# Performance work log

Measured on AMD Instinct MI355X. Metric: run time of the kernel, lower is better.

The kernel has to match this reference:

```python
import jax, jax.numpy as jnp
import numpy as np

EPS = 1e-6
NEG_SLOPE = 0.2


def setup_inputs() -> dict:
    key = jax.random.key(0)
    k1, k2 = jax.random.split(key)
    B, D, T = 4, 512, 2048
    H, Dh = 8, 512 // 8
    x = jax.random.normal(k1, (B, D, T), dtype=jnp.float32)
    qkv = jax.random.normal(k2, (3, H, D, Dh), dtype=jnp.float32) * 0.02
    norm_w = jnp.ones((1,), dtype=jnp.float32)
    return {"x": x, "qkv": qkv, "norm_w": norm_w}


def reference(x, qkv, norm_w):
    B, D, T = x.shape
    H = qkv.shape[1]
    # leaky relu on channels-first input
    x = jnp.where(x >= 0, x, NEG_SLOPE * x)
    # fused QKV projection: (B,D,T),(3,H,D,Dh) -> (3,B,H,T,Dh)
    h = jnp.einsum('bdt,nhdD->nbhtD', x, qkv)
    # RMSNorm over the sequence axis (dim=-2), scalar learned weight
    denom = jnp.mean(h * h, axis=-2, keepdims=True)
    h = norm_w * (h / jnp.sqrt(denom + EPS))
    q, k, v = h[0], h[1], h[2]
    scale = jnp.sqrt(jnp.asarray(D // H, dtype=x.dtype))
    # manual attention: (B,H,T,T) score matrix
    attn = jax.nn.softmax(jnp.einsum('bhtD,bhTD->bhtT', q, k) / scale, axis=-1)
    # weighted values, output laid out (B,H,Dh,T) then merged to (B,D,T)
    out = jnp.einsum('bhtT,bhTD->bhDt', attn, v)
    return out.reshape(B, D, T)
```

## Files before the change

### kernel.cpp

```cpp
#include <hip/hip_runtime.h>
#include <cstddef>

#define B   4
#define D   512
#define T   2048
#define H   8
#define DH  64
#define NEG_SLOPE 0.2f
#define EPS 1e-6f
#define LOG2E 1.44269504088896340736f

typedef __attribute__((ext_vector_type(8))) short short8;
typedef __attribute__((ext_vector_type(4))) float float4v;

__device__ __forceinline__ float bf2f(ushort u) {
    unsigned int x = ((unsigned int)u) << 16;
    return __builtin_bit_cast(float, x);
}
__device__ __forceinline__ ushort f2bf(float f) {
    unsigned int x = __builtin_bit_cast(unsigned int, f);
    x = x + 0x7fffu + ((x >> 16) & 1u);
    return (ushort)(x >> 16);
}

__global__ __launch_bounds__(256) void transpose_fused(const float* __restrict__ x,
                                                       const float* __restrict__ qkv,
                                                       ushort* __restrict__ xT,
                                                       ushort* __restrict__ WT,
                                                       float* __restrict__ ssq, int zcount) {
    const int tid = threadIdx.x;
    const int z = blockIdx.z;
    if (z == 0 && blockIdx.x == 0 && blockIdx.y == 0) {
        for (int i = tid; i < zcount; i += 256) ssq[i] = 0.f;
    }

    const float* s;
    ushort* d;
    int src_ld, dst_ld, do_lrelu;
    if (z < B) {
        const int c0 = blockIdx.x * 64, r0 = blockIdx.y * 64;
        s = x + (size_t)z * D * T + (size_t)r0 * T + c0;
        d = xT + (size_t)z * T * D + (size_t)c0 * D + r0;
        src_ld = T; dst_ld = D; do_lrelu = 1;
    } else {
        if (blockIdx.x != 0) return;
        const int g = z - B;
        const int r0 = blockIdx.y * 64;
        s = qkv + (size_t)g * D * DH + (size_t)r0 * DH;
        d = WT + (size_t)g * DH * D + r0;
        src_ld = DH; dst_ld = D; do_lrelu = 0;
    }

    __shared__ float Ls[64][68];
    const int rl = tid >> 4, c4 = (tid & 15) * 4;
    #pragma unroll
    for (int p = 0; p < 4; ++p) {
        float4 v = *(const float4*)(s + (size_t)(rl + p * 16) * src_ld + c4);
        if (do_lrelu) {
            v.x = fmaxf(v.x, NEG_SLOPE * v.x);
            v.y = fmaxf(v.y, NEG_SLOPE * v.y);
            v.z = fmaxf(v.z, NEG_SLOPE * v.z);
            v.w = fmaxf(v.w, NEG_SLOPE * v.w);
        }
        *(float4*)&Ls[rl + p * 16][c4] = v;
    }
    __syncthreads();

    const int tl = tid >> 2;
    #pragma unroll
    for (int it = 0; it < 2; ++it) {
        int ch = (tid & 3) + it * 4;
        ushort o[8];
        #pragma unroll
        for (int j = 0; j < 8; ++j) o[j] = f2bf(Ls[ch * 8 + j][tl]);
        *(uint4*)(d + (size_t)tl * dst_ld + ch * 8) = *(uint4*)o;
    }
}

__global__ __launch_bounds__(256) void qkv_mm(const ushort* __restrict__ xT,
                                              const ushort* __restrict__ WT,
                                              ushort* __restrict__ hb,
                                              ushort* __restrict__ vT,
                                              float* __restrict__ ssq) {
    const int tid = threadIdx.x, wave = tid >> 6, lane = tid & 63;
    const int quad = lane >> 4, l16 = lane & 15;
    const int wr = wave >> 1, wc = wave & 1;
    const int t0  = blockIdx.x * 128;
    const int gd0 = blockIdx.y * 128;
    const int b   = blockIdx.z;

    __shared__ ushort SMEM[4 * 8192];

    const ushort* xb = xT + (size_t)b * T * D + (size_t)t0 * D;
    const ushort* wb = WT + (size_t)gd0 * D;

    const int srow = lane >> 3;
    const int csrc = (lane & 7) ^ srow;
    const bool is_v = (blockIdx.y >= 8);

    float4v acc[4][4];
    #pragma unroll
    for (int i = 0; i < 4; ++i)
        #pragma unroll
        for (int j = 0; j < 4; ++j) acc[i][j] = (float4v){0.f, 0.f, 0.f, 0.f};

    {
        ushort* At = SMEM;
        ushort* Bt = SMEM + 8192;
        #pragma unroll
        for (int i = 0; i < 4; ++i) {
            int rbase = wave * 32 + i * 8;
            int row = rbase + srow;
            __builtin_amdgcn_global_load_lds(
                (const __attribute__((address_space(1))) unsigned int*)(xb + (size_t)row * D + csrc * 8),
                (__attribute__((address_space(3))) unsigned int*)&At[rbase * 64], 16, 0, 0);
            __builtin_amdgcn_global_load_lds(
                (const __attribute__((address_space(1))) unsigned int*)(wb + (size_t)row * D + csrc * 8),
                (__attribute__((address_space(3))) unsigned int*)&Bt[rbase * 64], 16, 0, 0);
        }
    }

    for (int ks = 0; ks < 8; ++ks) {
        __syncthreads();
        if (ks < 7) {
            int k0 = (ks + 1) * 64;
            ushort* At = SMEM + ((ks + 1) & 1) * 16384;
            ushort* Bt = At + 8192;
            #pragma unroll
            for (int i = 0; i < 4; ++i) {
                int rbase = wave * 32 + i * 8;
                int row = rbase + srow;
                __builtin_amdgcn_global_load_lds(
                    (const __attribute__((address_space(1))) unsigned int*)(xb + (size_t)row * D + k0 + csrc * 8),
                    (__attribute__((address_space(3))) unsigned int*)&At[rbase * 64], 16, 0, 0);
                __builtin_amdgcn_global_load_lds(
                    (const __attribute__((address_space(1))) unsigned int*)(wb + (size_t)row * D + k0 + csrc * 8),
                    (__attribute__((address_space(3))) unsigned int*)&Bt[rbase * 64], 16, 0, 0);
            }
        }
        const ushort* At = SMEM + (ks & 1) * 16384;
        const ushort* Bt = At + 8192;
        const ushort* Asrc = is_v ? At : Bt;
        const ushort* Bsrc = is_v ? Bt : At;
        const int arow0 = is_v ? wr * 64 : wc * 64;
        const int brow0 = is_v ? wc * 64 : wr * 64;

        #pragma unroll
        for (int kh = 0; kh < 2; ++kh) {
            short8 aF[4], bF[4];
            #pragma unroll
            for (int mt = 0; mt < 4; ++mt) {
                int row = arow0 + mt * 16 + l16;
                aF[mt] = *(const short8*)&Asrc[row * 64 + (((kh * 4 + quad) ^ (l16 & 7)) * 8)];
            }
            #pragma unroll
            for (int nt = 0; nt < 4; ++nt) {
                int row = brow0 + nt * 16 + l16;
                bF[nt] = *(const short8*)&Bsrc[row * 64 + (((kh * 4 + quad) ^ (l16 & 7)) * 8)];
            }
            #pragma unroll
            for (int mt = 0; mt < 4; ++mt)
                #pragma unroll
                for (int nt = 0; nt < 4; ++nt)
                    acc[mt][nt] = __builtin_amdgcn_mfma_f32_16x16x32_bf16(
                        aF[mt], bF[nt], acc[mt][nt], 0, 0, 0);
        }
    }

    const int g  = blockIdx.y * 2 + wc;
    const int n  = g >> 3, hh = g & 7;
    const int ch = ((n * B + b) * H + hh) * 64;
    ushort* E = SMEM + wave * 4096;

    #pragma unroll
    for (int mt = 0; mt < 4; ++mt) {
        #pragma unroll
        for (int nt = 0; nt < 4; ++nt) {
            float4v c = acc[mt][nt];
            ushort4 pk;
            pk.x = f2bf(c[0]); pk.y = f2bf(c[1]);
            pk.z = f2bf(c[2]); pk.w = f2bf(c[3]);
            int row   = nt * 16 + l16;
            int chunk = mt * 2 + (quad >> 1);
            int pos   = chunk ^ (l16 & 7);
            *(ushort4*)&E[row * 64 + pos * 8 + (quad & 1) * 4] = pk;
        }
    }

    const int rsub = lane >> 3;
    const int csub = lane & 7;
    const int posr = csub ^ rsub;

    if (!is_v) {
        ushort* hbase = hb + (((size_t)n * B + b) * H + hh) * (size_t)T * DH
                        + (size_t)(t0 + wr * 64) * DH;
        float sq8[8] = {0.f, 0.f, 0.f, 0.f, 0.f, 0.f, 0.f, 0.f};
        #pragma unroll
        for (int i = 0; i < 8; ++i) {
            uint4 v = *(const uint4*)&E[(i * 8 + rsub) * 64 + posr * 8];
            const ushort* u = (const ushort*)&v;
            #pragma unroll
            for (int j = 0; j < 8; ++j) { float f = bf2f(u[j]); sq8[j] += f * f; }
            *(uint4*)(hbase + (size_t)(i * 8 + rsub) * DH + csub * 8) = v;
        }
        #pragma unroll
        for (int j = 0; j < 8; ++j) {
            float s = sq8[j];
            s += __shfl_xor(s, 8); s += __shfl_xor(s, 16); s += __shfl_xor(s, 32);
            if (lane < 8) atomicAdd(&ssq[ch + lane * 8 + j], s);
        }
    } else {
        ushort* vbase = vT + ((size_t)b * H + hh) * (size_t)DH * T + (t0 + wr * 64);
        #pragma unroll
        for (int i = 0; i < 8; ++i) {
            uint4 v = *(const uint4*)&E[(i * 8 + rsub) * 64 + posr * 8];
            const ushort* u = (const ushort*)&v;
            float s = 0.f;
            #pragma unroll
            for (int j = 0; j < 8; ++j) { float f = bf2f(u[j]); s += f * f; }
            *(uint4*)(vbase + (size_t)(i * 8 + rsub) * T + csub * 8) = v;
            s += __shfl_xor(s, 1); s += __shfl_xor(s, 2); s += __shfl_xor(s, 4);
            if ((lane & 7) == 0) atomicAdd(&ssq[ch + i * 8 + rsub], s);
        }
    }
}

__global__ __launch_bounds__(256) void flash_attn(const ushort* __restrict__ hb,
                                                  const ushort* __restrict__ vT,
                                                  const float* __restrict__ ssq,
                                                  const float* __restrict__ norm_w,
                                                  float* __restrict__ out) {
    const int tid  = threadIdx.x;
    const int wave = tid >> 6;
    const int lane = tid & 63;
    const int quad = lane >> 4;
    const int l16  = lane & 15;

    const int lin  = blockIdx.x;
    const int head = ((lin & 7) << 2) | ((lin >> 3) & 3);
    const int t0   = (lin >> 5) * 128;
    const int b    = head >> 3, hh = head & 7;

    const size_t slab = (size_t)B * H * T * DH;
    const ushort* qp = hb + (size_t)head * T * DH;
    const ushort* kp = hb + slab + (size_t)head * T * DH;
    const ushort* vp = vT + (size_t)head * DH * T;

    __shared__ ushort Kt[2][64 * 64];
    __shared__ ushort Vt[2][64 * 64];
    __shared__ ushort Pb[4][32 * 64];
    __shared__ float fqk[64], sv[64];

    if (tid < 64) {
        float nw = norm_w[0];
        float mq = ssq[(0 * B * H + head) * 64 + tid] * (1.0f / T) + EPS;
        float mk = ssq[(1 * B * H + head) * 64 + tid] * (1.0f / T) + EPS;
        float mv = ssq[(2 * B * H + head) * 64 + tid] * (1.0f / T) + EPS;
        fqk[tid] = nw * nw * rsqrtf(mq) * rsqrtf(mk) * 0.125f * LOG2E;
        sv[tid]  = nw * rsqrtf(mv);
    }
    __syncthreads();

    short8 bQ[2][2];
    #pragma unroll
    for (int qg = 0; qg < 2; ++qg) {
        const ushort* qr = qp + (size_t)(t0 + wave * 32 + qg * 16 + l16) * DH;
        #pragma unroll
        for (int kh = 0; kh < 2; ++kh) {
            short8 raw = *(const short8*)(qr + kh * 32 + quad * 8);
            #pragma unroll
            for (int j = 0; j < 8; ++j) {
                float f = bf2f((ushort)raw[j]) * fqk[kh * 32 + quad * 8 + j];
                bQ[qg][kh][j] = (short)f2bf(f);
            }
        }
    }

    const int srow = lane >> 3;
    const int csrc = (lane & 7) ^ srow;
    const ushort* kA = kp + (size_t)(wave * 16 + srow) * DH + csrc * 8;
    const ushort* kB = kp + (size_t)(wave * 16 + 8 + srow) * DH + csrc * 8;
    const ushort* vA = vp + (size_t)(wave * 16 + srow) * T + csrc * 8;
    const ushort* vB = vp + (size_t)(wave * 16 + 8 + srow) * T + csrc * 8;

    float l_run[2] = {0.f, 0.f};
    float4v O[2][4];
    #pragma unroll
    for (int qg = 0; qg < 2; ++qg)
        #pragma unroll
        for (int dt = 0; dt < 4; ++dt) O[qg][dt] = (float4v){0.f, 0.f, 0.f, 0.f};

    {
        __builtin_amdgcn_global_load_lds(
            (const __attribute__((address_space(1))) unsigned int*)kA,
            (__attribute__((address_space(3))) unsigned int*)&Kt[0][(wave * 16) * 64], 16, 0, 0);
        __builtin_amdgcn_global_load_lds(
            (const __attribute__((address_space(1))) unsigned int*)kB,
            (__attribute__((address_space(3))) unsigned int*)&Kt[0][(wave * 16 + 8) * 64], 16, 0, 0);
        __builtin_amdgcn_global_load_lds(
            (const __attribute__((address_space(1))) unsigned int*)vA,
            (__attribute__((address_space(3))) unsigned int*)&Vt[0][(wave * 16) * 64], 16, 0, 0);
        __builtin_amdgcn_global_load_lds(
            (const __attribute__((address_space(1))) unsigned int*)vB,
            (__attribute__((address_space(3))) unsigned int*)&Vt[0][(wave * 16 + 8) * 64], 16, 0, 0);
    }

    for (int jt = 0; jt < 32; ++jt) {
        __syncthreads();
        if (jt < 31) {
            const int p = (jt + 1) & 1;
            const size_t jk = (size_t)(jt + 1) * 64;
            __builtin_amdgcn_global_load_lds(
                (const __attribute__((address_space(1))) unsigned int*)(kA + jk * DH),
                (__attribute__((address_space(3))) unsigned int*)&Kt[p][(wave * 16) * 64], 16, 0, 0);
            __builtin_amdgcn_global_load_lds(
                (const __attribute__((address_space(1))) unsigned int*)(kB + jk * DH),
                (__attribute__((address_space(3))) unsigned int*)&Kt[p][(wave * 16 + 8) * 64], 16, 0, 0);
            __builtin_amdgcn_global_load_lds(
                (const __attribute__((address_space(1))) unsigned int*)(vA + jk),
                (__attribute__((address_space(3))) unsigned int*)&Vt[p][(wave * 16) * 64], 16, 0, 0);
            __builtin_amdgcn_global_load_lds(
                (const __attribute__((address_space(1))) unsigned int*)(vB + jk),
                (__attribute__((address_space(3))) unsigned int*)&Vt[p][(wave * 16 + 8) * 64], 16, 0, 0);
        }
        const int p = jt & 1;

        float4v S[2][4];
        #pragma unroll
        for (int qg = 0; qg < 2; ++qg)
            #pragma unroll
            for (int mt = 0; mt < 4; ++mt) S[qg][mt] = (float4v){0.f, 0.f, 0.f, 0.f};
        #pragma unroll
        for (int kh = 0; kh < 2; ++kh) {
            #pragma unroll
            for (int mt = 0; mt < 4; ++mt) {
                int row = mt * 16 + l16;
                short8 aK = *(const short8*)&Kt[p][row * 64 + (((kh * 4 + quad) ^ (row & 7)) * 8)];
                #pragma unroll
                for (int qg = 0; qg < 2; ++qg)
                    S[qg][mt] = __builtin_amdgcn_mfma_f32_16x16x32_bf16(aK, bQ[qg][kh], S[qg][mt], 0, 0, 0);
            }
        }

        #pragma unroll
        for (int qg = 0; qg < 2; ++qg) {
            #pragma unroll
            for (int mt = 0; mt < 4; ++mt) {
                float p0 = __builtin_amdgcn_exp2f(S[qg][mt][0]);
                float p1 = __builtin_amdgcn_exp2f(S[qg][mt][1]);
                float p2 = __builtin_amdgcn_exp2f(S[qg][mt][2]);
                float p3 = __builtin_amdgcn_exp2f(S[qg][mt][3]);
                l_run[qg] += (p0 + p1) + (p2 + p3);
                unsigned int a0 = __builtin_bit_cast(unsigned int, p0) + 0x8000u;
                unsigned int a1 = __builtin_bit_cast(unsigned int, p1) + 0x8000u;
                unsigned int a2 = __builtin_bit_cast(unsigned int, p2) + 0x8000u;
                unsigned int a3 = __builtin_bit_cast(unsigned int, p3) + 0x8000u;
                uint2 pk;
                pk.x = __builtin_amdgcn_perm(a1, a0, 0x07060302u);
                pk.y = __builtin_amdgcn_perm(a3, a2, 0x07060302u);
                *(uint2*)&Pb[wave][(qg * 16 + l16) * 64
                                   + (((mt * 2 + (quad >> 1)) ^ (l16 & 7)) * 8)
                                   + (quad & 1) * 4] = pk;
            }
        }

        #pragma unroll
        for (int kh = 0; kh < 2; ++kh) {
            short8 bP[2];
            #pragma unroll
            for (int qg = 0; qg < 2; ++qg)
                bP[qg] = *(const short8*)&Pb[wave][(qg * 16 + l16) * 64
                                                   + (((kh * 4 + quad) ^ (l16 & 7)) * 8)];
            #pragma unroll
            for (int dt = 0; dt < 4; ++dt) {
                int row = dt * 16 + l16;
                short8 aV = *(const short8*)&Vt[p][row * 64 + (((kh * 4 + quad) ^ (row & 7)) * 8)];
                #pragma unroll
                for (int qg = 0; qg < 2; ++qg)
                    O[qg][dt] = __builtin_amdgcn_mfma_f32_16x16x32_bf16(aV, bP[qg], O[qg][dt], 0, 0, 0);
            }
        }
    }

    #pragma unroll
    for (int qg = 0; qg < 2; ++qg) {
        float rs = l_run[qg];
        rs += __shfl_xor(rs, 16);
        rs += __shfl_xor(rs, 32);
        float inv = 1.f / rs;
        const int t = t0 + wave * 32 + qg * 16 + l16;
        #pragma unroll
        for (int dt = 0; dt < 4; ++dt) {
            #pragma unroll
            for (int r = 0; r < 4; ++r) {
                int dd = dt * 16 + quad * 4 + r;
                out[((size_t)b * D + hh * DH + dd) * T + t] = O[qg][dt][r] * inv * sv[dd];
            }
        }
    }
}

extern "C" void kernel_launch(void* const* d_in, const int* in_sizes, int n_in,
                              void* d_out, int out_size, void* d_ws, size_t ws_size,
                              hipStream_t stream) {
    const float* x      = (const float*)d_in[0];
    const float* qkv    = (const float*)d_in[1];
    const float* norm_w = (const float*)d_in[2];
    float* out = (float*)d_out;

    const size_t HB_BYTES = (size_t)2 * B * H * T * DH * 2;
    const size_t VT_BYTES = (size_t)B * H * DH * T * 2;
    const size_t XT_BYTES = (size_t)B * T * D * 2;
    const size_t WT_BYTES = (size_t)3 * H * DH * D * 2;
    ushort* hb  = (ushort*)d_ws;
    ushort* vT  = (ushort*)((char*)d_ws + HB_BYTES);
    ushort* xT  = (ushort*)((char*)d_ws + HB_BYTES + VT_BYTES);
    ushort* WT  = (ushort*)((char*)d_ws + HB_BYTES + VT_BYTES + XT_BYTES);
    float*  ssq = (float*)((char*)d_ws + HB_BYTES + VT_BYTES + XT_BYTES + WT_BYTES);
    const int SSQ_N = 3 * B * H * DH;

    transpose_fused<<<dim3(T / 64, D / 64, B + 3 * H), 256, 0, stream>>>(
        x, qkv, xT, WT, ssq, SSQ_N);
    qkv_mm<<<dim3(T / 128, (3 * H * DH) / 128, B), 256, 0, stream>>>(xT, WT, hb, vT, ssq);
    flash_attn<<<dim3((T / 128) * B * H), 256, 0, stream>>>(hb, vT, ssq, norm_w, out);
}
```

Measured before the change: 171.0 us.

## Keep softmax probabilities in registers for PV MFMA; single-buffer QKV GEMM LDS

In the attention kernel, the exponentiated scores are no longer written to and re-read from a per-wave LDS buffer. They are bit-cast straight into operands for 16x16x16 bf16 MFMAs whose K dimension matches the score accumulator layout, and V fragments are read from LDS in the matching 4-element layout. This removes an LDS round trip and frees LDS, at the cost of twice as many smaller MFMA instructions. Separately, the QKV GEMM drops double-buffered LDS in favour of a single buffer with two barriers per k-step, trading load/compute overlap for lower LDS use and likely higher occupancy.

New measurement: 164.0 us. 1.04x faster.

```diff
diff --git a/kernel.cpp b/kernel.cpp
--- a/kernel.cpp
+++ b/kernel.cpp
@@ -11,6 +11,7 @@
 #define LOG2E 1.44269504088896340736f
 
 typedef __attribute__((ext_vector_type(8))) short short8;
+typedef __attribute__((ext_vector_type(4))) short sh4;
 typedef __attribute__((ext_vector_type(4))) float float4v;
 
 __device__ __forceinline__ float bf2f(ushort u) {
@@ -89,7 +90,9 @@
     const int gd0 = blockIdx.y * 128;
     const int b   = blockIdx.z;
 
-    __shared__ ushort SMEM[4 * 8192];
+    __shared__ ushort SMEM[2 * 128 * 64];
+    ushort* At = SMEM;
+    ushort* Bt = SMEM + 128 * 64;
 
     const ushort* xb = xT + (size_t)b * T * D + (size_t)t0 * D;
     const ushort* wb = WT + (size_t)gd0 * D;
@@ -97,6 +100,10 @@
     const int srow = lane >> 3;
     const int csrc = (lane & 7) ^ srow;
     const bool is_v = (blockIdx.y >= 8);
+    const ushort* Asrc = is_v ? At : Bt;
+    const ushort* Bsrc = is_v ? Bt : At;
+    const int arow0 = is_v ? wr * 64 : wc * 64;
+    const int brow0 = is_v ? wc * 64 : wr * 64;
 
     float4v acc[4][4];
     #pragma unroll
@@ -104,46 +111,19 @@
         #pragma unroll
         for (int j = 0; j < 4; ++j) acc[i][j] = (float4v){0.f, 0.f, 0.f, 0.f};
 
-    {
-        ushort* At = SMEM;
-        ushort* Bt = SMEM + 8192;
+    for (int k0 = 0; k0 < D; k0 += 64) {
         #pragma unroll
         for (int i = 0; i < 4; ++i) {
             int rbase = wave * 32 + i * 8;
             int row = rbase + srow;
             __builtin_amdgcn_global_load_lds(
-                (const __attribute__((address_space(1))) unsigned int*)(xb + (size_t)row * D + csrc * 8),
+                (const __attribute__((address_space(1))) unsigned int*)(xb + (size_t)row * D + k0 + csrc * 8),
                 (__attribute__((address_space(3))) unsigned int*)&At[rbase * 64], 16, 0, 0);
             __builtin_amdgcn_global_load_lds(
-                (const __attribute__((address_space(1))) unsigned int*)(wb + (size_t)row * D + csrc * 8),
+                (const __attribute__((address_space(1))) unsigned int*)(wb + (size_t)row * D + k0 + csrc * 8),
                 (__attribute__((address_space(3))) unsigned int*)&Bt[rbase * 64], 16, 0, 0);
         }
-    }
-
-    for (int ks = 0; ks < 8; ++ks) {
         __syncthreads();
-        if (ks < 7) {
-            int k0 = (ks + 1) * 64;
-            ushort* At = SMEM + ((ks + 1) & 1) * 16384;
-            ushort* Bt = At + 8192;
-            #pragma unroll
-            for (int i = 0; i < 4; ++i) {
-                int rbase = wave * 32 + i * 8;
-                int row = rbase + srow;
-                __builtin_amdgcn_global_load_lds(
-                    (const __attribute__((address_space(1))) unsigned int*)(xb + (size_t)row * D + k0 + csrc * 8),
-                    (__attribute__((address_space(3))) unsigned int*)&At[rbase * 64], 16, 0, 0);
-                __builtin_amdgcn_global_load_lds(
-                    (const __attribute__((address_space(1))) unsigned int*)(wb + (size_t)row * D + k0 + csrc * 8),
-                    (__attribute__((address_space(3))) unsigned int*)&Bt[rbase * 64], 16, 0, 0);
-            }
-        }
-        const ushort* At = SMEM + (ks & 1) * 16384;
-        const ushort* Bt = At + 8192;
-        const ushort* Asrc = is_v ? At : Bt;
-        const ushort* Bsrc = is_v ? Bt : At;
-        const int arow0 = is_v ? wr * 64 : wc * 64;
-        const int brow0 = is_v ? wc * 64 : wr * 64;
 
         #pragma unroll
         for (int kh = 0; kh < 2; ++kh) {
@@ -165,6 +145,7 @@
                     acc[mt][nt] = __builtin_amdgcn_mfma_f32_16x16x32_bf16(
                         aF[mt], bF[nt], acc[mt][nt], 0, 0, 0);
         }
+        __syncthreads();
     }
 
     const int g  = blockIdx.y * 2 + wc;
@@ -248,7 +229,6 @@
 
     __shared__ ushort Kt[2][64 * 64];
     __shared__ ushort Vt[2][64 * 64];
-    __shared__ ushort Pb[4][32 * 64];
     __shared__ float fqk[64], sv[64];
 
     if (tid < 64) {
@@ -290,38 +270,36 @@
         #pragma unroll
         for (int dt = 0; dt < 4; ++dt) O[qg][dt] = (float4v){0.f, 0.f, 0.f, 0.f};
 
-    {
-        __builtin_amdgcn_global_load_lds(
-            (const __attribute__((address_space(1))) unsigned int*)kA,
-            (__attribute__((address_space(3))) unsigned int*)&Kt[0][(wave * 16) * 64], 16, 0, 0);
-        __builtin_amdgcn_global_load_lds(
-            (const __attribute__((address_space(1))) unsigned int*)kB,
-            (__attribute__((address_space(3))) unsigned int*)&Kt[0][(wave * 16 + 8) * 64], 16, 0, 0);
-        __builtin_amdgcn_global_load_lds(
-            (const __attribute__((address_space(1))) unsigned int*)vA,
-            (__attribute__((address_space(3))) unsigned int*)&Vt[0][(wave * 16) * 64], 16, 0, 0);
-        __builtin_amdgcn_global_load_lds(
-            (const __attribute__((address_space(1))) unsigned int*)vB,
-            (__attribute__((address_space(3))) unsigned int*)&Vt[0][(wave * 16 + 8) * 64], 16, 0, 0);
-    }
+    __builtin_amdgcn_global_load_lds(
+        (const __attribute__((address_space(1))) unsigned int*)kA,
+        (__attribute__((address_space(3))) unsigned int*)&Kt[0][(wave * 16) * 64], 16, 0, 0);
+    __builtin_amdgcn_global_load_lds(
+        (const __attribute__((address_space(1))) unsigned int*)kB,
+        (__attribute__((address_space(3))) unsigned int*)&Kt[0][(wave * 16 + 8) * 64], 16, 0, 0);
+    __builtin_amdgcn_global_load_lds(
+        (const __attribute__((address_space(1))) unsigned int*)vA,
+        (__attribute__((address_space(3))) unsigned int*)&Vt[0][(wave * 16) * 64], 16, 0, 0);
+    __builtin_amdgcn_global_load_lds(
+        (const __attribute__((address_space(1))) unsigned int*)vB,
+        (__attribute__((address_space(3))) unsigned int*)&Vt[0][(wave * 16 + 8) * 64], 16, 0, 0);
 
     for (int jt = 0; jt < 32; ++jt) {
         __syncthreads();
         if (jt < 31) {
-            const int p = (jt + 1) & 1;
+            const int pn = (jt + 1) & 1;
             const size_t jk = (size_t)(jt + 1) * 64;
             __builtin_amdgcn_global_load_lds(
                 (const __attribute__((address_space(1))) unsigned int*)(kA + jk * DH),
-                (__attribute__((address_space(3))) unsigned int*)&Kt[p][(wave * 16) * 64], 16, 0, 0);
+                (__attribute__((address_space(3))) unsigned int*)&Kt[pn][(wave * 16) * 64], 16, 0, 0);
             __builtin_amdgcn_global_load_lds(
                 (const __attribute__((address_space(1))) unsigned int*)(kB + jk * DH),
-                (__attribute__((address_space(3))) unsigned int*)&Kt[p][(wave * 16 + 8) * 64], 16, 0, 0);
+                (__attribute__((address_space(3))) unsigned int*)&Kt[pn][(wave * 16 + 8) * 64], 16, 0, 0);
             __builtin_amdgcn_global_load_lds(
                 (const __attribute__((address_space(1))) unsigned int*)(vA + jk),
-                (__attribute__((address_space(3))) unsigned int*)&Vt[p][(wave * 16) * 64], 16, 0, 0);
+                (__attribute__((address_space(3))) unsigned int*)&Vt[pn][(wave * 16) * 64], 16, 0, 0);
             __builtin_amdgcn_global_load_lds(
                 (const __attribute__((address_space(1))) unsigned int*)(vB + jk),
-                (__attribute__((address_space(3))) unsigned int*)&Vt[p][(wave * 16 + 8) * 64], 16, 0, 0);
+                (__attribute__((address_space(3))) unsigned int*)&Vt[pn][(wave * 16 + 8) * 64], 16, 0, 0);
         }
         const int p = jt & 1;
 
@@ -342,6 +320,7 @@
             }
         }
 
+        sh4 bP[2][4];
         #pragma unroll
         for (int qg = 0; qg < 2; ++qg) {
             #pragma unroll
@@ -358,26 +337,21 @@
                 uint2 pk;
                 pk.x = __builtin_amdgcn_perm(a1, a0, 0x07060302u);
                 pk.y = __builtin_amdgcn_perm(a3, a2, 0x07060302u);
-                *(uint2*)&Pb[wave][(qg * 16 + l16) * 64
-                                   + (((mt * 2 + (quad >> 1)) ^ (l16 & 7)) * 8)
-                                   + (quad & 1) * 4] = pk;
-            }
-        }
-
-        #pragma unroll
-        for (int kh = 0; kh < 2; ++kh) {
-            short8 bP[2];
-            #pragma unroll
-            for (int qg = 0; qg < 2; ++qg)
-                bP[qg] = *(const short8*)&Pb[wave][(qg * 16 + l16) * 64
-                                                   + (((kh * 4 + quad) ^ (l16 & 7)) * 8)];
+                bP[qg][mt] = __builtin_bit_cast(sh4, pk);
+            }
+        }
+
+        #pragma unroll
+        for (int mt = 0; mt < 4; ++mt) {
             #pragma unroll
             for (int dt = 0; dt < 4; ++dt) {
-                int row = dt * 16 + l16;
-                short8 aV = *(const short8*)&Vt[p][row * 64 + (((kh * 4 + quad) ^ (row & 7)) * 8)];
+                int dd = dt * 16 + l16;
+                sh4 aV = *(const sh4*)&Vt[p][dd * 64 + (((mt * 2 + (quad >> 1)) ^ (dd & 7)) * 8)
+                                            + (quad & 1) * 4];
                 #pragma unroll
                 for (int qg = 0; qg < 2; ++qg)
-                    O[qg][dt] = __builtin_amdgcn_mfma_f32_16x16x32_bf16(aV, bP[qg], O[qg][dt], 0, 0, 0);
+                    O[qg][dt] = __builtin_amdgcn_mfma_f32_16x16x16bf16_1k(
+                        aV, bP[qg][mt], O[qg][dt], 0, 0, 0);
             }
         }
     }
```
